# Kernel tuning notes

Measured on AMD Instinct MI355X. Metric: run time of the kernel, lower is better.

The kernel has to match this reference:

```python
import jax, jax.numpy as jnp
import numpy as np

B, T, D, H = 2, 2048, 1024, 16
NEG = -65504.0


def setup_inputs() -> dict:
    key = jax.random.key(0)
    ks = jax.random.split(key, 12)
    std = float(np.sqrt(2.0 / (D + D)))  # xavier_normal for square weights
    inp = {
        'q': jax.random.normal(ks[0], (B, T, D), jnp.float32),
        'k': jax.random.normal(ks[1], (B, T, D), jnp.float32),
        'v': jax.random.normal(ks[2], (B, T, D), jnp.float32),
        'mask': jax.random.randint(ks[3], (B, T), 0, 2, jnp.int32),
        # weights stored as (in, out) so y = x @ W + b
        'Wq': jax.random.normal(ks[4], (D, D), jnp.float32) * std,
        'bq': jnp.zeros((D,), jnp.float32),
        'Wk': jax.random.normal(ks[5], (D, D), jnp.float32) * std,
        'bk': jnp.zeros((D,), jnp.float32),
        'Wv': jax.random.normal(ks[6], (D, D), jnp.float32) * std,
        'bv': jnp.zeros((D,), jnp.float32),
        'Wo': jax.random.normal(ks[7], (D, D), jnp.float32) * std,
        'bo': jnp.zeros((D,), jnp.float32),
    }
    return inp


def reference(q, k, v, mask, Wq, bq, Wk, bk, Wv, bv, Wo, bo):
    b, t, _ = q.shape
    dim_a = Wq.shape[1]
    dh = dim_a // H
    # projections, then split into heads: (b, t, H, dh)
    qh = (q @ Wq + bq).reshape(b, t, H, dh)
    kh = (k @ Wk + bk).reshape(b, t, H, dh)
    vh = (v @ Wv + bv).reshape(b, t, H, dh)
    # NOTE: module scales by 1/sqrt(dim_a) with the FULL dim_a, not per-head
    a = jnp.einsum('bthd,bshd->bhts', qh, kh) / jnp.sqrt(jnp.float32(dim_a))
    # 2D mask broadcasts over query positions: (b, 1, 1, t_keys)
    a = jnp.where(mask[:, None, None, :] == 0, NEG, a)
    a = jax.nn.softmax(a, axis=-1)  # dropout_prob=0 (eval mode)
    o = jnp.einsum('bhts,bshd->bthd', a, vh).reshape(b, t, dim_a)
    return o @ Wo + bo
```

## Files before the change

### kernel.cpp

```cpp
#include <hip/hip_runtime.h>
#include <hip/hip_bf16.h>
#include <math.h>

#define B_ 2
#define T_ 2048
#define D_ 1024
#define H_ 16
#define QSCALE (0.03125f * 1.44269504088896f)

typedef _Float16 f16;
using f16x4 = __attribute__((ext_vector_type(4))) _Float16;
using f16x8 = __attribute__((ext_vector_type(8))) _Float16;
using f32x4 = __attribute__((ext_vector_type(4))) float;

__device__ __forceinline__ void gl16(const void* g, void* l) {
  __builtin_amdgcn_global_load_lds(
      (__attribute__((address_space(1))) void*)g,
      (__attribute__((address_space(3))) void*)l, 16, 0, 0);
}

__global__ __launch_bounds__(256) void prep(
    const float* __restrict__ q, const float* __restrict__ k,
    const float* __restrict__ v, const int* __restrict__ mask,
    const float* __restrict__ Wq, const float* __restrict__ Wk,
    const float* __restrict__ Wv, const float* __restrict__ Wo,
    const float* __restrict__ bq, const float* __restrict__ bk,
    const float* __restrict__ bv, const float* __restrict__ bo,
    f16* __restrict__ xqkv, f16* __restrict__ Wt, float* __restrict__ bias,
    int* __restrict__ idx, int* __restrict__ inv, int* __restrict__ nk,
    f16* __restrict__ khc) {
  __shared__ float sh[64][65];
  const int bid = blockIdx.x;
  const int tid = threadIdx.x;

  if (bid < 6144) {
    const int z = bid / 2048;
    const float* src = (z == 0) ? q : (z == 1) ? k : v;
    const size_t i = ((size_t)(bid % 2048) * 256 + tid) * 8;
    float4 a = *(const float4*)(src + i);
    float4 b = *(const float4*)(src + i + 4);
    f16x8 o;
    o[0] = (f16)a.x; o[1] = (f16)a.y; o[2] = (f16)a.z; o[3] = (f16)a.w;
    o[4] = (f16)b.x; o[5] = (f16)b.y; o[6] = (f16)b.z; o[7] = (f16)b.w;
    *(f16x8*)(xqkv + (size_t)z * 4194304 + i) = o;
  } else if (bid < 7168) {
    const int id = bid - 6144;
    const int z = id >> 8;
    const int k0 = ((id >> 4) & 15) * 64, n0 = (id & 15) * 64;
    const float* W = (z == 0) ? Wq : (z == 1) ? Wk : (z == 2) ? Wv : Wo;
    const int r = tid >> 2, c0 = (tid & 3) * 16;
#pragma unroll
    for (int i = 0; i < 4; ++i)
      *(float4*)&sh[r][c0 + 4 * i] =
          *(const float4*)&W[(size_t)(k0 + r) * 1024 + n0 + c0 + 4 * i];
    __syncthreads();
    f16 tmp[16];
#pragma unroll
    for (int i = 0; i < 16; ++i) tmp[i] = (f16)sh[c0 + i][r];
    f16* dst = Wt + (size_t)z * 1048576 + (size_t)(n0 + r) * 1024 + k0 + c0;
    *(f16x8*)dst = *(f16x8*)&tmp[0];
    *(f16x8*)(dst + 8) = *(f16x8*)&tmp[8];
  } else if (bid < 7184) {
    const int i = (bid - 7168) * 256 + tid;
    const int z = i >> 10;
    const float* s = (z == 0) ? bq : (z == 1) ? bk : (z == 2) ? bv : bo;
    bias[i] = s[i & 1023];
  } else {
    const int b = bid - 7184;
    int* cnt = (int*)sh;
    int loc[8];
    int c = 0;
#pragma unroll
    for (int i = 0; i < 8; ++i) {
      loc[i] = mask[b * T_ + tid * 8 + i];
      c += loc[i];
    }
    cnt[tid] = c;
    __syncthreads();
    for (int off = 1; off < 256; off <<= 1) {
      int vsh = (tid >= off) ? cnt[tid - off] : 0;
      __syncthreads();
      cnt[tid] += vsh;
      __syncthreads();
    }
    int pos = cnt[tid] - c;
#pragma unroll
    for (int i = 0; i < 8; ++i) {
      const int t = tid * 8 + i;
      if (loc[i]) {
        idx[b * T_ + pos] = t;
        inv[b * T_ + t] = pos;
        ++pos;
      } else {
        inv[b * T_ + t] = -1;
      }
    }
    const int n = cnt[255];
    if (tid == 255) nk[b] = n;
    const int nkt = (n + 63) >> 6;
    const int npadrows = (nkt << 6) - n;
    uint4 z4 = {0u, 0u, 0u, 0u};
    f16* base = khc + ((size_t)b * T_ + n) * D_;
    for (int i = tid; i < npadrows * 128; i += 256)
      *(uint4*)(base + (size_t)i * 8) = z4;
  }
}

template <int TM, typename OT>
__global__ __launch_bounds__(256) void gemm_bt(
    const f16* __restrict__ Xb, const f16* __restrict__ Wtb,
    const float* __restrict__ biasb, void* __restrict__ C0,
    void* __restrict__ C1, void* __restrict__ C2,
    const int* __restrict__ inv, int M, int N, int K, float qscale) {
  constexpr int FM = TM / 32;
  __shared__ __align__(16) f16 As[TM * 32];
  __shared__ __align__(16) f16 Bs[128 * 32];
  const int z = blockIdx.z;
  const f16* X  = Xb  + (size_t)z * M * K;
  const f16* Wt = Wtb + (size_t)z * N * K;
  const float* bias = biasb + (size_t)z * N;
  OT* C = (OT*)((z == 0) ? C0 : (z == 1) ? C1 : C2);
  const float scl = (z == 0) ? qscale : 1.f;

  const int tid = threadIdx.x;
  const int wave = tid >> 6, lane = tid & 63;
  const int quad = lane >> 4, l16 = lane & 15;
  const int wm = wave & 1, wn = wave >> 1;
  const int m0 = blockIdx.y * TM, n0 = blockIdx.x * 128;

  f32x4 acc[FM][4] = {};

  const f16* asrc = X  + (size_t)(m0 + (tid >> 2)) * K + (tid & 3) * 8;
  const f16* bsrc = Wt + (size_t)(n0 + (tid >> 2)) * K + (tid & 3) * 8;
  char* aldst = (char*)As + tid * 16;
  char* bldst = (char*)Bs + tid * 16;
  const size_t rstep = (size_t)64 * K;

  const int NK = K >> 5;
  for (int kt = 0; kt < NK; ++kt) {
    if (kt) __syncthreads();
    gl16(asrc, aldst);
    if constexpr (TM == 128) gl16(asrc + rstep, aldst + 4096);
    gl16(bsrc, bldst);
    gl16(bsrc + rstep, bldst + 4096);
    asrc += 32; bsrc += 32;
    __syncthreads();

    f16x8 af[FM], bf[4];
#pragma unroll
    for (int t = 0; t < FM; ++t)
      af[t] = *(const f16x8*)&As[((TM / 2) * wm + 16 * t + l16) * 32 + quad * 8];
#pragma unroll
    for (int t = 0; t < 4; ++t)
      bf[t] = *(const f16x8*)&Bs[(64 * wn + 16 * t + l16) * 32 + quad * 8];
#pragma unroll
    for (int i = 0; i < FM; ++i)
#pragma unroll
      for (int j = 0; j < 4; ++j)
        acc[i][j] = __builtin_amdgcn_mfma_f32_16x16x32_f16(af[i], bf[j], acc[i][j], 0, 0, 0);
  }

  const int cm = m0 + (TM / 2) * wm + 4 * quad;
  const int cn = n0 + 64 * wn + l16;
  float bv[4];
#pragma unroll
  for (int tn = 0; tn < 4; ++tn) bv[tn] = bias[cn + 16 * tn];

  if (inv != nullptr && z == 1) {
    const int bb = m0 >> 11;
#pragma unroll
    for (int tm = 0; tm < FM; ++tm) {
#pragma unroll
      for (int r = 0; r < 4; ++r) {
        const int m = cm + 16 * tm + r;
        const int j = inv[m];
        if (j >= 0) {
          OT* row = C + ((size_t)(bb << 11) + j) * N;
#pragma unroll
          for (int tn = 0; tn < 4; ++tn)
            row[cn + 16 * tn] = (OT)(acc[tm][tn][r] + bv[tn]);
        }
      }
    }
  } else {
#pragma unroll
    for (int tm = 0; tm < FM; ++tm)
#pragma unroll
      for (int r = 0; r < 4; ++r) {
        OT* row = C + (size_t)(cm + 16 * tm + r) * N;
#pragma unroll
        for (int tn = 0; tn < 4; ++tn)
          row[cn + 16 * tn] = (OT)((acc[tm][tn][r] + bv[tn]) * scl);
      }
  }
}

__global__ __launch_bounds__(256) void vtrans(
    const f16* __restrict__ vh, const int* __restrict__ idx,
    const int* __restrict__ nk, f16* __restrict__ vhT) {
  const int tt = blockIdx.x, bh = blockIdx.y;
  const int b = bh >> 4, h = bh & 15;
  const int n = nk[b];
  const int nkt = (n + 63) >> 6;
  if (tt >= nkt) return;
  __shared__ f16 t[64][72];
  const int tid = threadIdx.x;
  const int r = tid >> 2, cq = 16 * (tid & 3);

  const int j = tt * 64 + r;
  uint4 v0 = {0u, 0u, 0u, 0u}, v1 = {0u, 0u, 0u, 0u};
  if (j < n) {
    const int tsrc = idx[b * T_ + j];
    const uint4* src = (const uint4*)(vh + ((size_t)b * T_ + tsrc) * D_ + h * 64 + cq);
    v0 = src[0]; v1 = src[1];
  }
  *(uint4*)&t[r][cq]     = v0;
  *(uint4*)&t[r][cq + 8] = v1;
  __syncthreads();

  f16 tmp[16];
#pragma unroll
  for (int xx = 0; xx < 16; ++xx) {
    int x = (xx + r) & 15;
    tmp[x] = t[cq + x][r];
  }
  f16* dst = vhT + ((size_t)bh * 64 + r) * T_ + tt * 64 + cq;
  *(uint4*)&dst[0] = *(uint4*)&tmp[0];
  *(uint4*)&dst[8] = *(uint4*)&tmp[8];
}

__global__ __launch_bounds__(256) void attn_mfma(
    const f16* __restrict__ qh, const f16* __restrict__ khc,
    const f16* __restrict__ vhT, const int* __restrict__ nkd,
    f16* __restrict__ oat) {
  __shared__ f16 Ks[64][72];
  __shared__ f16 Vt[64][72];
  __shared__ f16 Ps[4][32][72];

  const int qt = blockIdx.x, bh = blockIdx.y;
  const int b = bh >> 4, h = bh & 15;
  const int tid = threadIdx.x;
  const int wave = tid >> 6, lane = tid & 63;
  const int quad = lane >> 4, l16 = lane & 15;
  const int sr = tid >> 2, sq = 16 * (tid & 3);

  const int n = nkd[b];
  const int nkt = (n + 63) >> 6;
  const int npad = (nkt << 6) - n;

  f16x8 qf[2][2];
#pragma unroll
  for (int gq = 0; gq < 2; ++gq) {
    const f16* qp = qh + ((size_t)(b * T_ + qt * 128 + wave * 32 + 16 * gq + l16)) * D_ + h * 64 + quad * 8;
    qf[gq][0] = *(const f16x8*)qp;
    qf[gq][1] = *(const f16x8*)(qp + 32);
  }

  float lsum[2] = {0.f, 0.f};
  f32x4 o[2][4] = {};

  const f16* kbase = khc + (size_t)b * T_ * D_ + h * 64;
  const f16* vbase = vhT + ((size_t)bh * 64 + sr) * T_;

  uint4 kr0, kr1, vr0, vr1;
  auto load_kv = [&](int kt) {
    const uint4* ks = (const uint4*)(kbase + (size_t)(kt * 64 + sr) * D_ + sq);
    kr0 = ks[0]; kr1 = ks[1];
    const uint4* vs = (const uint4*)(vbase + kt * 64 + sq);
    vr0 = vs[0]; vr1 = vs[1];
  };
  if (nkt > 0) load_kv(0);

  for (int kt = 0; kt < nkt; ++kt) {
    *(uint4*)&Ks[sr][sq]     = kr0;
    *(uint4*)&Ks[sr][sq + 8] = kr1;
    *(uint4*)&Vt[sr][sq]     = vr0;
    *(uint4*)&Vt[sr][sq + 8] = vr1;
    __syncthreads();
    if (kt + 1 < nkt) load_kv(kt + 1);

#pragma unroll
    for (int tn = 0; tn < 4; ++tn) {
      f16x8 kf0 = *(const f16x8*)&Ks[16 * tn + l16][quad * 8];
      f16x8 kf1 = *(const f16x8*)&Ks[16 * tn + l16][32 + quad * 8];
#pragma unroll
      for (int gq = 0; gq < 2; ++gq) {
        f32x4 s = {0.f, 0.f, 0.f, 0.f};
        s = __builtin_amdgcn_mfma_f32_16x16x32_f16(kf0, qf[gq][0], s, 0, 0, 0);
        s = __builtin_amdgcn_mfma_f32_16x16x32_f16(kf1, qf[gq][1], s, 0, 0, 0);
        float p0 = exp2f(s[0]), p1 = exp2f(s[1]);
        float p2 = exp2f(s[2]), p3 = exp2f(s[3]);
        lsum[gq] += (p0 + p1) + (p2 + p3);
        f16x4 pk;
        pk[0] = (f16)p0; pk[1] = (f16)p1; pk[2] = (f16)p2; pk[3] = (f16)p3;
        *(f16x4*)&Ps[wave][16 * gq + l16][16 * tn + 4 * quad] = pk;
      }
    }

    f16x8 pf[2][2];
#pragma unroll
    for (int gq = 0; gq < 2; ++gq) {
      pf[gq][0] = *(const f16x8*)&Ps[wave][16 * gq + l16][quad * 8];
      pf[gq][1] = *(const f16x8*)&Ps[wave][16 * gq + l16][32 + quad * 8];
    }
#pragma unroll
    for (int t = 0; t < 4; ++t) {
      f16x8 vf0 = *(const f16x8*)&Vt[16 * t + l16][quad * 8];
      f16x8 vf1 = *(const f16x8*)&Vt[16 * t + l16][32 + quad * 8];
#pragma unroll
      for (int gq = 0; gq < 2; ++gq) {
        o[gq][t] = __builtin_amdgcn_mfma_f32_16x16x32_f16(pf[gq][0], vf0, o[gq][t], 0, 0, 0);
        o[gq][t] = __builtin_amdgcn_mfma_f32_16x16x32_f16(pf[gq][1], vf1, o[gq][t], 0, 0, 0);
      }
    }
    __syncthreads();
  }

#pragma unroll
  for (int gq = 0; gq < 2; ++gq) {
    float ls = lsum[gq];
    ls += __shfl_xor(ls, 16);
    ls += __shfl_xor(ls, 32);
    ls -= (float)npad;
    const size_t orow = (size_t)(b * T_ + qt * 128 + wave * 32 + 16 * gq + 4 * quad);
#pragma unroll
    for (int r = 0; r < 4; ++r) {
      const float iv = 1.f / __shfl(ls, 4 * quad + r);
#pragma unroll
      for (int t = 0; t < 4; ++t)
        oat[(orow + r) * D_ + h * 64 + 16 * t + l16] = (f16)(o[gq][t][r] * iv);
    }
  }
}

extern "C" void kernel_launch(void* const* d_in, const int* in_sizes, int n_in,
                              void* d_out, int out_size, void* d_ws, size_t ws_size,
                              hipStream_t stream) {
  const float* q  = (const float*)d_in[0];
  const float* k  = (const float*)d_in[1];
  const float* v  = (const float*)d_in[2];
  const int* mask = (const int*)d_in[3];
  const float* Wq = (const float*)d_in[4];
  const float* bq = (const float*)d_in[5];
  const float* Wk = (const float*)d_in[6];
  const float* bk = (const float*)d_in[7];
  const float* Wv = (const float*)d_in[8];
  const float* bv = (const float*)d_in[9];
  const float* Wo = (const float*)d_in[10];
  const float* bo = (const float*)d_in[11];
  float* out = (float*)d_out;

  char* ws = (char*)d_ws;
  f16* xqkv  = (f16*)(ws);
  f16* Wt    = (f16*)(ws + 25165824);
  f16* qh    = (f16*)(ws + 33554432);
  f16* vh    = (f16*)(ws + 41943040);
  f16* khc   = (f16*)(ws + 50331648);
  float* bsw = (float*)(ws + 58720256);
  int* idx   = (int*)(ws + 58736640);
  int* inv   = (int*)(ws + 58753024);
  int* nk    = (int*)(ws + 58769408);
  f16* vhT   = (f16*)(ws);
  f16* oat   = (f16*)(ws + 8388608);

  const int M = B_ * T_;
  dim3 blk(256);

  prep<<<dim3(7186), blk, 0, stream>>>(q, k, v, mask, Wq, Wk, Wv, Wo,
                                       bq, bk, bv, bo, xqkv, Wt, bsw,
                                       idx, inv, nk, khc);

  gemm_bt<128, f16><<<dim3(8, 32, 3), blk, 0, stream>>>(
      xqkv, Wt, bsw, qh, khc, vh, inv, M, D_, D_, QSCALE);

  vtrans<<<dim3(32, 32), blk, 0, stream>>>(vh, idx, nk, vhT);

  attn_mfma<<<dim3(16, 32), blk, 0, stream>>>(qh, khc, vhT, nk, oat);

  gemm_bt<64, float><<<dim3(8, 64, 1), blk, 0, stream>>>(
      oat, Wt + 3145728, bsw + 3072, out, out, out, nullptr, M, D_, D_, 1.f);
}
```

Measured before the change: 236.0 us.

## Use 8 waves of 16 query rows each in attention instead of 4 waves of 32

The attention kernel now launches 512 threads per block, and each wave handles 16 query rows instead of 32. The K/V tile loads are spread over twice as many threads, so each thread loads one 16-byte chunk per tile. This halves per-thread accumulators and registers and raises wave-level parallelism to hide latency. In exchange, each wave reuses a loaded K/V fragment over fewer MFMAs, so LDS read traffic per FLOP doubles.

```diff
diff --git a/kernel.cpp b/kernel.cpp
--- a/kernel.cpp
+++ b/kernel.cpp
@@ -229,53 +229,48 @@
   *(uint4*)&dst[8] = *(uint4*)&tmp[8];
 }
 
-__global__ __launch_bounds__(256) void attn_mfma(
+__global__ __launch_bounds__(512) void attn_mfma(
     const f16* __restrict__ qh, const f16* __restrict__ khc,
     const f16* __restrict__ vhT, const int* __restrict__ nkd,
     f16* __restrict__ oat) {
   __shared__ f16 Ks[64][72];
   __shared__ f16 Vt[64][72];
-  __shared__ f16 Ps[4][32][72];
+  __shared__ f16 Ps[8][16][72];
 
   const int qt = blockIdx.x, bh = blockIdx.y;
   const int b = bh >> 4, h = bh & 15;
   const int tid = threadIdx.x;
   const int wave = tid >> 6, lane = tid & 63;
   const int quad = lane >> 4, l16 = lane & 15;
-  const int sr = tid >> 2, sq = 16 * (tid & 3);
+  const int sr = tid >> 3, sq = 8 * (tid & 7);
 
   const int n = nkd[b];
   const int nkt = (n + 63) >> 6;
   const int npad = (nkt << 6) - n;
 
-  f16x8 qf[2][2];
-#pragma unroll
-  for (int gq = 0; gq < 2; ++gq) {
-    const f16* qp = qh + ((size_t)(b * T_ + qt * 128 + wave * 32 + 16 * gq + l16)) * D_ + h * 64 + quad * 8;
-    qf[gq][0] = *(const f16x8*)qp;
-    qf[gq][1] = *(const f16x8*)(qp + 32);
-  }
-
-  float lsum[2] = {0.f, 0.f};
-  f32x4 o[2][4] = {};
+  f16x8 qf[2];
+  {
+    const f16* qp = qh + ((size_t)(b * T_ + qt * 128 + wave * 16 + l16)) * D_ + h * 64 + quad * 8;
+    qf[0] = *(const f16x8*)qp;
+    qf[1] = *(const f16x8*)(qp + 32);
+  }
+
+  float lsum = 0.f;
+  f32x4 o[4] = {};
 
   const f16* kbase = khc + (size_t)b * T_ * D_ + h * 64;
   const f16* vbase = vhT + ((size_t)bh * 64 + sr) * T_;
 
-  uint4 kr0, kr1, vr0, vr1;
+  uint4 kr, vr;
   auto load_kv = [&](int kt) {
-    const uint4* ks = (const uint4*)(kbase + (size_t)(kt * 64 + sr) * D_ + sq);
-    kr0 = ks[0]; kr1 = ks[1];
-    const uint4* vs = (const uint4*)(vbase + kt * 64 + sq);
-    vr0 = vs[0]; vr1 = vs[1];
+    kr = *(const uint4*)(kbase + (size_t)(kt * 64 + sr) * D_ + sq);
+    vr = *(const uint4*)(vbase + kt * 64 + sq);
   };
   if (nkt > 0) load_kv(0);
 
   for (int kt = 0; kt < nkt; ++kt) {
-    *(uint4*)&Ks[sr][sq]     = kr0;
-    *(uint4*)&Ks[sr][sq + 8] = kr1;
-    *(uint4*)&Vt[sr][sq]     = vr0;
-    *(uint4*)&Vt[sr][sq + 8] = vr1;
+    *(uint4*)&Ks[sr][sq] = kr;
+    *(uint4*)&Vt[sr][sq] = vr;
     __syncthreads();
     if (kt + 1 < nkt) load_kv(kt + 1);
 
@@ -283,52 +278,41 @@
     for (int tn = 0; tn < 4; ++tn) {
       f16x8 kf0 = *(const f16x8*)&Ks[16 * tn + l16][quad * 8];
       f16x8 kf1 = *(const f16x8*)&Ks[16 * tn + l16][32 + quad * 8];
-#pragma unroll
-      for (int gq = 0; gq < 2; ++gq) {
-        f32x4 s = {0.f, 0.f, 0.f, 0.f};
-        s = __builtin_amdgcn_mfma_f32_16x16x32_f16(kf0, qf[gq][0], s, 0, 0, 0);
-        s = __builtin_amdgcn_mfma_f32_16x16x32_f16(kf1, qf[gq][1], s, 0, 0, 0);
-        float p0 = exp2f(s[0]), p1 = exp2f(s[1]);
-        float p2 = exp2f(s[2]), p3 = exp2f(s[3]);
-        lsum[gq] += (p0 + p1) + (p2 + p3);
-        f16x4 pk;
-        pk[0] = (f16)p0; pk[1] = (f16)p1; pk[2] = (f16)p2; pk[3] = (f16)p3;
-        *(f16x4*)&Ps[wave][16 * gq + l16][16 * tn + 4 * quad] = pk;
-      }
-    }
-
-    f16x8 pf[2][2];
-#pragma unroll
-    for (int gq = 0; gq < 2; ++gq) {
-      pf[gq][0] = *(const f16x8*)&Ps[wave][16 * gq + l16][quad * 8];
-      pf[gq][1] = *(const f16x8*)&Ps[wave][16 * gq + l16][32 + quad * 8];
-    }
+      f32x4 s = {0.f, 0.f, 0.f, 0.f};
+      s = __builtin_amdgcn_mfma_f32_16x16x32_f16(kf0, qf[0], s, 0, 0, 0);
+      s = __builtin_amdgcn_mfma_f32_16x16x32_f16(kf1, qf[1], s, 0, 0, 0);
+      float p0 = exp2f(s[0]), p1 = exp2f(s[1]);
+      float p2 = exp2f(s[2]), p3 = exp2f(s[3]);
+      lsum += (p0 + p1) + (p2 + p3);
+      f16x4 pk;
+      pk[0] = (f16)p0; pk[1] = (f16)p1; pk[2] = (f16)p2; pk[3] = (f16)p3;
+      *(f16x4*)&Ps[wave][l16][16 * tn + 4 * quad] = pk;
+    }
+
+    f16x8 pf0 = *(const f16x8*)&Ps[wave][l16][quad * 8];
+    f16x8 pf1 = *(const f16x8*)&Ps[wave][l16][32 + quad * 8];
 #pragma unroll
     for (int t = 0; t < 4; ++t) {
       f16x8 vf0 = *(const f16x8*)&Vt[16 * t + l16][quad * 8];
       f16x8 vf1 = *(const f16x8*)&Vt[16 * t + l16][32 + quad * 8];
-#pragma unroll
-      for (int gq = 0; gq < 2; ++gq) {
-        o[gq][t] = __builtin_amdgcn_mfma_f32_16x16x32_f16(pf[gq][0], vf0, o[gq][t], 0, 0, 0);
-        o[gq][t] = __builtin_amdgcn_mfma_f32_16x16x32_f16(pf[gq][1], vf1, o[gq][t], 0, 0, 0);
-      }
-    }
-    __syncthreads();
-  }
-
-#pragma unroll
-  for (int gq = 0; gq < 2; ++gq) {
-    float ls = lsum[gq];
+      o[t] = __builtin_amdgcn_mfma_f32_16x16x32_f16(pf0, vf0, o[t], 0, 0, 0);
+      o[t] = __builtin_amdgcn_mfma_f32_16x16x32_f16(pf1, vf1, o[t], 0, 0, 0);
+    }
+    __syncthreads();
+  }
+
+  {
+    float ls = lsum;
     ls += __shfl_xor(ls, 16);
     ls += __shfl_xor(ls, 32);
     ls -= (float)npad;
-    const size_t orow = (size_t)(b * T_ + qt * 128 + wave * 32 + 16 * gq + 4 * quad);
+    const size_t orow = (size_t)(b * T_ + qt * 128 + wave * 16 + 4 * quad);
 #pragma unroll
     for (int r = 0; r < 4; ++r) {
       const float iv = 1.f / __shfl(ls, 4 * quad + r);
 #pragma unroll
       for (int t = 0; t < 4; ++t)
-        oat[(orow + r) * D_ + h * 64 + 16 * t + l16] = (f16)(o[gq][t][r] * iv);
+        oat[(orow + r) * D_ + h * 64 + 16 * t + l16] = (f16)(o[t][r] * iv);
     }
   }
 }
@@ -375,7 +359,7 @@
 
   vtrans<<<dim3(32, 32), blk, 0, stream>>>(vh, idx, nk, vhT);
 
-  attn_mfma<<<dim3(16, 32), blk, 0, stream>>>(qh, khc, vhT, nk, oat);
+  attn_mfma<<<dim3(16, 32), dim3(512), 0, stream>>>(qh, khc, vhT, nk, oat);
 
   gemm_bt<64, float><<<dim3(8, 64, 1), blk, 0, stream>>>(
       oat, Wt + 3145728, bsw + 3072, out, out, out, nullptr, M, D_, D_, 1.f);
```

New measurement: 230.7 us. 1.02x faster.
